# Kernel tuning notes

Measured on AMD Instinct MI355X. Metric: run time of the kernel, lower is better.

Reference implementation:

```python
import jax, jax.numpy as jnp
import numpy as np

NUM_USER = 50000
NUM_ITEM = 50000
NUM_NODES = NUM_USER + NUM_ITEM
DIM_LATENT = 256
DIM_ID = 64
NUM_EDGES = 2_000_000


def setup_inputs() -> dict:
    key = jax.random.key(0)
    ks = jax.random.split(key, 16)
    xn = lambda k, shape, s: (jax.random.normal(k, shape, dtype=jnp.float32) * s)
    # xavier-normal-ish std for [in,out] weights
    def xavier(k, fan_in, fan_out):
        std = float(np.sqrt(2.0 / (fan_in + fan_out)))
        return jax.random.normal(k, (fan_in, fan_out), dtype=jnp.float32) * std
    edge_index = jax.random.randint(ks[0], (2, NUM_EDGES), 0, NUM_NODES, dtype=jnp.int64)
    return {
        "features": xn(ks[1], (NUM_ITEM, DIM_LATENT), 1.0),
        "id_embedding": xn(ks[2], (NUM_NODES, DIM_ID), 1.0),
        "preference": xn(ks[3], (NUM_USER, DIM_LATENT), 0.1),
        "W_gcn0": xavier(ks[4], DIM_LATENT, DIM_ID),
        "W_gcn1": xavier(ks[5], DIM_ID, DIM_ID),
        "lin_w0": xavier(ks[6], DIM_LATENT, DIM_ID),
        "lin_b0": jnp.zeros((DIM_ID,), jnp.float32),
        "lin_w1": xavier(ks[7], DIM_ID, DIM_ID),
        "lin_b1": jnp.zeros((DIM_ID,), jnp.float32),
        "g_w0": xavier(ks[8], DIM_ID, DIM_ID),
        "g_b0": jnp.zeros((DIM_ID,), jnp.float32),
        "g_w1": xavier(ks[9], DIM_ID, DIM_ID),
        "g_b1": jnp.zeros((DIM_ID,), jnp.float32),
        "edge_index": edge_index,
    }


def _gcn(x, W, row, col, norm):
    # H = scatter_add(row, (x W)[col] * norm)
    h = x @ W                                  # [N, out]
    msg = h[col] * norm[:, None]               # [E, out] gather + scale
    return jax.ops.segment_sum(msg, row, num_segments=NUM_NODES)


def reference(features, id_embedding, preference, W_gcn0, W_gcn1,
              lin_w0, lin_b0, lin_w1, lin_b1, g_w0, g_b0, g_w1, g_b1,
              edge_index):
    row, col = edge_index[0], edge_index[1]
    # degree normalization: deg from scatter_add of ones over row
    deg = jax.ops.segment_sum(jnp.ones((row.shape[0],), jnp.float32), row,
                              num_segments=NUM_NODES)
    deg = jnp.maximum(deg, 1.0)
    dis = deg ** -0.5
    norm = dis[row] * dis[col]                 # [E]

    x = jnp.concatenate([preference, features], axis=0)   # [N, dim_latent]
    x = x / jnp.maximum(jnp.linalg.norm(x, axis=1, keepdims=True), 1e-12)

    lrelu = jax.nn.leaky_relu  # slope 0.01, matches torch default
    for W_gcn, lin_w, lin_b, g_w, g_b in (
        (W_gcn0, lin_w0, lin_b0, g_w0, g_b0),
        (W_gcn1, lin_w1, lin_b1, g_w1, g_b1),
    ):
        h = lrelu(_gcn(x, W_gcn, row, col, norm))          # [N, dim_id]
        x_hat = lrelu(x @ lin_w + lin_b) + id_embedding    # has_id=True
        x = lrelu(h @ g_w + g_b + x_hat)                   # concate=False
    return x
```

## Files before the change

kernel.cpp:

```cpp
#include <hip/hip_runtime.h>

#define NUM_USER   50000
#define NUM_ITEM   50000
#define NUM_NODES  100000
#define DIM_LATENT 256
#define DIM_ID     64
#define NUM_EDGES  2000000
#define NBUCKET    391
#define BPB        8192
#define NCHUNK     245
#define HSTRIDE    392

typedef __attribute__((ext_vector_type(8))) short bf8_t;
typedef __attribute__((ext_vector_type(4))) float f4_t;
typedef __attribute__((ext_vector_type(2))) float f2_t;

static __device__ __forceinline__ float lrelu(float x) {
    return x > 0.0f ? x : 0.01f * x;
}
static __device__ __forceinline__ unsigned short f2bf(float f) {
    unsigned u = __float_as_uint(f);
    u += 0x7fff + ((u >> 16) & 1);
    return (unsigned short)(u >> 16);
}
static __device__ __forceinline__ float bf2f(unsigned short u) {
    return __uint_as_float(((unsigned)u) << 16);
}
static __device__ __forceinline__ float bflo(unsigned u) {
    return __uint_as_float(u << 16);
}
static __device__ __forceinline__ float bfhi(unsigned u) {
    return __uint_as_float(u & 0xffff0000u);
}

__global__ void __launch_bounds__(256, 8) k_xnorm(const float* __restrict__ pref,
                                                  const float* __restrict__ feat,
                                                  unsigned short* __restrict__ xn) {
    const int w = threadIdx.x >> 6;
    const int lane = threadIdx.x & 63;
    const int n = blockIdx.x * 4 + w;
    const float* src = (n < NUM_USER) ? (pref + (size_t)n * DIM_LATENT)
                                      : (feat + (size_t)(n - NUM_USER) * DIM_LATENT);
    float4 v = reinterpret_cast<const float4*>(src)[lane];
    float ss = v.x*v.x + v.y*v.y + v.z*v.z + v.w*v.w;
    #pragma unroll
    for (int off = 32; off >= 1; off >>= 1) ss += __shfl_xor(ss, off);
    float sc = 1.0f / fmaxf(sqrtf(ss), 1e-12f);
    ushort4 p;
    p.x = f2bf(v.x * sc); p.y = f2bf(v.y * sc);
    p.z = f2bf(v.z * sc); p.w = f2bf(v.w * sc);
    *reinterpret_cast<ushort4*>(&xn[(size_t)n * DIM_LATENT + lane * 4]) = p;
}

__global__ void __launch_bounds__(256) k_hist(const int* __restrict__ row,
                                              int* __restrict__ hist) {
    __shared__ int lh[NBUCKET];
    const int g = blockIdx.x, t = threadIdx.x;
    for (int i = t; i < NBUCKET; i += 256) lh[i] = 0;
    __syncthreads();
    const int base = g * BPB;
    for (int i = 0; i < BPB; i += 256) {
        int e = base + i + t;
        if (e < NUM_EDGES) atomicAdd(&lh[row[e] >> 8], 1);
    }
    __syncthreads();
    for (int i = t; i < NBUCKET; i += 256) hist[g * HSTRIDE + i] = lh[i];
}

__global__ void __launch_bounds__(256) k_off1(int* __restrict__ hist,
                                              int* __restrict__ bcnt) {
    __shared__ int wsum[4];
    const int b = blockIdx.x, t = threadIdx.x;
    const int lane = t & 63, w = t >> 6;
    int c = (t < NCHUNK) ? hist[t * HSTRIDE + b] : 0;
    int v = c;
    #pragma unroll
    for (int off = 1; off < 64; off <<= 1) {
        int u = __shfl_up(v, off);
        if (lane >= off) v += u;
    }
    if (lane == 63) wsum[w] = v;
    __syncthreads();
    int add = 0;
    #pragma unroll
    for (int i = 0; i < 4; ++i) if (i < w) add += wsum[i];
    int incl = v + add;
    if (t < NCHUNK) hist[t * HSTRIDE + b] = incl - c;
    if (t == 255) bcnt[b] = incl;
}

__global__ void __launch_bounds__(512) k_bscan(const int* __restrict__ bcnt,
                                               int* __restrict__ boff) {
    __shared__ int wsum[8];
    const int t = threadIdx.x;
    const int lane = t & 63, w = t >> 6;
    int c = (t < NBUCKET) ? bcnt[t] : 0;
    int v = c;
    #pragma unroll
    for (int off = 1; off < 64; off <<= 1) {
        int u = __shfl_up(v, off);
        if (lane >= off) v += u;
    }
    if (lane == 63) wsum[w] = v;
    __syncthreads();
    int add = 0;
    #pragma unroll
    for (int i = 0; i < 8; ++i) if (i < w) add += wsum[i];
    int ex = v + add - c;
    if (t < NBUCKET) boff[t] = ex;
    if (t == NBUCKET - 1) boff[NBUCKET] = ex + c;
}

__global__ void __launch_bounds__(256) k_bin2(const int* __restrict__ row,
                                              const int* __restrict__ col,
                                              const int* __restrict__ hist,
                                              const int* __restrict__ boff,
                                              unsigned* __restrict__ epack) {
    __shared__ int curs[NBUCKET];
    const int g = blockIdx.x, t = threadIdx.x;
    for (int i = t; i < NBUCKET; i += 256) curs[i] = boff[i] + hist[g * HSTRIDE + i];
    __syncthreads();
    const int base = g * BPB;
    for (int i = 0; i < BPB; i += 256) {
        int e = base + i + t;
        if (e < NUM_EDGES) {
            int r = row[e];
            int pos = atomicAdd(&curs[r >> 8], 1);
            epack[pos] = ((unsigned)(r & 255) << 24) | (unsigned)col[e];
        }
    }
}

__global__ void __launch_bounds__(512) k_csr(const unsigned* __restrict__ epack,
                                             const int* __restrict__ boff,
                                             int* __restrict__ offs,
                                             int* __restrict__ cnt,
                                             float* __restrict__ dis,
                                             int* __restrict__ ecol) {
    __shared__ int lcnt[256];
    __shared__ int lofs[256];
    __shared__ int wsum[4];
    const int b = blockIdx.x, t = threadIdx.x;
    const int start = boff[b], end = boff[b + 1];
    if (t < 256) lcnt[t] = 0;
    __syncthreads();
    for (int e = start + t; e < end; e += 512)
        atomicAdd(&lcnt[epack[e] >> 24], 1);
    __syncthreads();

    const int lane = t & 63, w = t >> 6;
    int c = (t < 256) ? lcnt[t] : 0;
    int v = c;
    #pragma unroll
    for (int off = 1; off < 64; off <<= 1) {
        int u = __shfl_up(v, off);
        if (lane >= off) v += u;
    }
    if (t < 256 && lane == 63) wsum[w] = v;
    __syncthreads();
    if (t < 256) {
        int add = 0;
        #pragma unroll
        for (int i = 0; i < 4; ++i) if (i < w) add += wsum[i];
        int ex = v + add - c;
        lofs[t] = start + ex;
        int n = (b << 8) + t;
        if (n < NUM_NODES) {
            offs[n] = start + ex;
            cnt[n]  = c;
            dis[n]  = rsqrtf((float)max(c, 1));
        }
    }
    __syncthreads();
    for (int e = start + t; e < end; e += 512) {
        unsigned p = epack[e];
        int pos = atomicAdd(&lofs[p >> 24], 1);
        ecol[pos] = (int)(p & 0x00ffffffu);
    }
}

__global__ void __launch_bounds__(256) k_wprep(const float* __restrict__ Wg,
                                               const float* __restrict__ Wl,
                                               unsigned short* __restrict__ wfrag) {
    int g = blockIdx.x * 256 + threadIdx.x;
    if (g >= 4096) return;
    int ks = g >> 9;
    int t  = (g >> 6) & 7;
    int l  = g & 63;
    const float* W = (t < 4) ? Wg : Wl;
    int colg = (t & 3) * 16 + (l & 15);
    int kb = ks * 32 + (l >> 4) * 8;
    unsigned short o[8];
    #pragma unroll
    for (int e = 0; e < 8; ++e) o[e] = f2bf(W[(size_t)(kb + e) * DIM_ID + colg]);
    unsigned short* dst = wfrag + (size_t)g * 8;
    #pragma unroll
    for (int e = 0; e < 8; ++e) dst[e] = o[e];
}

__global__ void __launch_bounds__(256) k_wprep64(const float* __restrict__ W0,
                                                 const float* __restrict__ W1,
                                                 const float* __restrict__ W2,
                                                 const float* __restrict__ W3,
                                                 unsigned short* __restrict__ frag) {
    int g = blockIdx.x * 256 + threadIdx.x;
    if (g >= 2048) return;
    int m = g >> 9;
    int r = g & 511;
    int ks = r >> 8;
    int t  = (r >> 6) & 3;
    int l  = r & 63;
    const float* W = (m == 0) ? W0 : (m == 1) ? W1 : (m == 2) ? W2 : W3;
    int colg = t * 16 + (l & 15);
    int kb = ks * 32 + (l >> 4) * 8;
    unsigned short o[8];
    #pragma unroll
    for (int e = 0; e < 8; ++e) o[e] = f2bf(W[(size_t)(kb + e) * DIM_ID + colg]);
    unsigned short* dst = frag + (size_t)g * 8;
    #pragma unroll
    for (int e = 0; e < 8; ++e) dst[e] = o[e];
}

__global__ void __launch_bounds__(256, 3) k_l1(
    const unsigned short* __restrict__ xn,
    const unsigned short* __restrict__ wfrag,
    const float* __restrict__ lb,   const float* __restrict__ idemb,
    unsigned short* __restrict__ hbf, unsigned short* __restrict__ xhat)
{
    __shared__ unsigned short st[4][16][68];
    const int lane = threadIdx.x & 63;
    const int w = threadIdx.x >> 6;
    const int ql = lane & 15, q = lane >> 4;
    const int rowBase = (blockIdx.x * 4 + w) * 16;
    const int row = rowBase + ql;
    const unsigned short* src = xn + (size_t)((row < NUM_NODES) ? row : 0) * DIM_LATENT;

    bf8_t af[8];
    #pragma unroll
    for (int ks = 0; ks < 8; ++ks)
        af[ks] = *reinterpret_cast<const bf8_t*>(src + ks * 32 + q * 8);

    f4_t acc[8];
    #pragma unroll
    for (int t = 0; t < 8; ++t) acc[t] = (f4_t){0.f, 0.f, 0.f, 0.f};

    const bf8_t* wf = reinterpret_cast<const bf8_t*>(wfrag);
    #pragma unroll
    for (int ks = 0; ks < 8; ++ks) {
        #pragma unroll
        for (int t = 0; t < 8; ++t) {
            bf8_t b = wf[(ks * 8 + t) * 64 + lane];
            acc[t] = __builtin_amdgcn_mfma_f32_16x16x32_bf16(af[ks], b, acc[t], 0, 0, 0);
        }
    }

    #pragma unroll
    for (int t = 0; t < 4; ++t)
        #pragma unroll
        for (int reg = 0; reg < 4; ++reg)
            st[w][q * 4 + reg][t * 16 + ql] = f2bf(acc[t][reg]);
    #pragma unroll
    for (int it = 0; it < 4; ++it) {
        int i = it * 64 + lane;
        int r = i >> 4, c8 = i & 15;
        int n = rowBase + r;
        uint2 v = *reinterpret_cast<const uint2*>(&st[w][r][c8 * 4]);
        if (n < NUM_NODES)
            *reinterpret_cast<uint2*>(&hbf[(size_t)n * DIM_ID + c8 * 4]) = v;
    }

    #pragma unroll
    for (int t = 4; t < 8; ++t) {
        int colg = (t - 4) * 16 + ql;
        float lbl = lb[colg];
        #pragma unroll
        for (int reg = 0; reg < 4; ++reg)
            st[w][q * 4 + reg][colg] = f2bf(lrelu(acc[t][reg] + lbl));
    }
    #pragma unroll
    for (int it = 0; it < 4; ++it) {
        int i = it * 64 + lane;
        int r = i >> 4, c8 = i & 15;
        int n = rowBase + r;
        if (n < NUM_NODES) {
            uint2 s = *reinterpret_cast<const uint2*>(&st[w][r][c8 * 4]);
            float4 idv = *reinterpret_cast<const float4*>(&idemb[(size_t)n * DIM_ID + c8 * 4]);
            uint2 o;
            o.x = (unsigned)f2bf(bflo(s.x) + idv.x) | ((unsigned)f2bf(bfhi(s.x) + idv.y) << 16);
            o.y = (unsigned)f2bf(bflo(s.y) + idv.z) | ((unsigned)f2bf(bfhi(s.y) + idv.w) << 16);
            *reinterpret_cast<uint2*>(&xhat[(size_t)n * DIM_ID + c8 * 4]) = o;
        }
    }
}

__global__ void __launch_bounds__(256, 8) k_hcvt(const uint2* __restrict__ hp,
                                                 const float* __restrict__ dis,
                                                 unsigned* __restrict__ out) {
    int t = blockIdx.x * 256 + threadIdx.x;
    float dn = dis[t >> 4];
    uint2 u = hp[t];
    float v0 = bflo(u.x) * dn, v1 = bfhi(u.x) * dn;
    float v2 = bflo(u.y) * dn, v3 = bfhi(u.y) * dn;
    int p = __builtin_amdgcn_cvt_pk_fp8_f32(v0, v1, 0, false);
    p = __builtin_amdgcn_cvt_pk_fp8_f32(v2, v3, p, true);
    out[t] = (unsigned)p;
}

__global__ void __launch_bounds__(256, 8) k_hcvt1(const uint2* __restrict__ hp,
                                                  unsigned* __restrict__ out) {
    int t = blockIdx.x * 256 + threadIdx.x;
    uint2 u = hp[t];
    int p = __builtin_amdgcn_cvt_pk_fp8_f32(bflo(u.x), bfhi(u.x), 0, false);
    p = __builtin_amdgcn_cvt_pk_fp8_f32(bflo(u.y), bfhi(u.y), p, true);
    out[t] = (unsigned)p;
}

__global__ void __launch_bounds__(256, 8) k_gather(
    const unsigned char* __restrict__ hbf8, const float* __restrict__ dis,
    const int* __restrict__ offs, const int* __restrict__ cnt,
    const int* __restrict__ ecol, unsigned short* __restrict__ Hb)
{
    const int w = threadIdx.x >> 6;
    const int lane = threadIdx.x & 63;
    const int g = lane >> 3;
    const int k = lane & 7;
    const int n = blockIdx.x * 4 + w;

    const float dn = dis[n];
    const int start = offs[n];
    const int m = cnt[n];

    f2_t s01 = {0.f, 0.f}, s23 = {0.f, 0.f}, s45 = {0.f, 0.f}, s67 = {0.f, 0.f};

    for (int base = 0; base < m; base += 64) {
        int e = base + lane;
        int ec = (e < m) ? ecol[start + e] : 0;
        int lim = m - base; if (lim > 64) lim = 64;
        int nj = (lim + 7) >> 3;
        for (int jj = 0; jj < nj; jj += 4) {
            int i0 = jj * 8 + g, i1 = i0 + 8, i2 = i0 + 16, i3 = i0 + 24;
            int c0 = __shfl(ec, i0), c1 = __shfl(ec, i1);
            int c2 = __shfl(ec, i2), c3 = __shfl(ec, i3);
            uint2 u0 = make_uint2(0u,0u), u1 = make_uint2(0u,0u);
            uint2 u2 = make_uint2(0u,0u), u3 = make_uint2(0u,0u);
            if (i0 < lim) u0 = *reinterpret_cast<const uint2*>(hbf8 + (size_t)(c0 << 6) + (k << 3));
            if (i1 < lim) u1 = *reinterpret_cast<const uint2*>(hbf8 + (size_t)(c1 << 6) + (k << 3));
            if (i2 < lim) u2 = *reinterpret_cast<const uint2*>(hbf8 + (size_t)(c2 << 6) + (k << 3));
            if (i3 < lim) u3 = *reinterpret_cast<const uint2*>(hbf8 + (size_t)(c3 << 6) + (k << 3));
            s01 += __builtin_amdgcn_cvt_pk_f32_fp8(u0.x, false);
            s23 += __builtin_amdgcn_cvt_pk_f32_fp8(u0.x, true);
            s45 += __builtin_amdgcn_cvt_pk_f32_fp8(u0.y, false);
            s67 += __builtin_amdgcn_cvt_pk_f32_fp8(u0.y, true);
            s01 += __builtin_amdgcn_cvt_pk_f32_fp8(u1.x, false);
            s23 += __builtin_amdgcn_cvt_pk_f32_fp8(u1.x, true);
            s45 += __builtin_amdgcn_cvt_pk_f32_fp8(u1.y, false);
            s67 += __builtin_amdgcn_cvt_pk_f32_fp8(u1.y, true);
            s01 += __builtin_amdgcn_cvt_pk_f32_fp8(u2.x, false);
            s23 += __builtin_amdgcn_cvt_pk_f32_fp8(u2.x, true);
            s45 += __builtin_amdgcn_cvt_pk_f32_fp8(u2.y, false);
            s67 += __builtin_amdgcn_cvt_pk_f32_fp8(u2.y, true);
            s01 += __builtin_amdgcn_cvt_pk_f32_fp8(u3.x, false);
            s23 += __builtin_amdgcn_cvt_pk_f32_fp8(u3.x, true);
            s45 += __builtin_amdgcn_cvt_pk_f32_fp8(u3.y, false);
            s67 += __builtin_amdgcn_cvt_pk_f32_fp8(u3.y, true);
        }
    }
    float a0 = s01.x, a1 = s01.y, a2 = s23.x, a3 = s23.y;
    float a4 = s45.x, a5 = s45.y, a6 = s67.x, a7 = s67.y;
    #pragma unroll
    for (int off = 8; off <= 32; off <<= 1) {
        a0 += __shfl_xor(a0, off); a1 += __shfl_xor(a1, off);
        a2 += __shfl_xor(a2, off); a3 += __shfl_xor(a3, off);
        a4 += __shfl_xor(a4, off); a5 += __shfl_xor(a5, off);
        a6 += __shfl_xor(a6, off); a7 += __shfl_xor(a7, off);
    }
    if (lane < 8) {
        uint4 o;
        o.x = (unsigned)f2bf(a0 * dn) | ((unsigned)f2bf(a1 * dn) << 16);
        o.y = (unsigned)f2bf(a2 * dn) | ((unsigned)f2bf(a3 * dn) << 16);
        o.z = (unsigned)f2bf(a4 * dn) | ((unsigned)f2bf(a5 * dn) << 16);
        o.w = (unsigned)f2bf(a6 * dn) | ((unsigned)f2bf(a7 * dn) << 16);
        *reinterpret_cast<uint4*>(&Hb[(size_t)n * DIM_ID + lane * 8]) = o;
    }
}

__global__ void __launch_bounds__(256, 3) k_mid(
    const unsigned short* __restrict__ Hb, const unsigned short* __restrict__ xhat1,
    const unsigned short* __restrict__ wf64,
    const float* __restrict__ gb,  const float* __restrict__ lb1,
    const float* __restrict__ idemb, const float* __restrict__ dis,
    unsigned short* __restrict__ hbf, unsigned short* __restrict__ xhat2)
{
    __shared__ unsigned short x1s[4][16][DIM_ID];
    __shared__ unsigned short st[4][16][68];
    const int lane = threadIdx.x & 63;
    const int w = threadIdx.x >> 6;
    const int ql = lane & 15, q = lane >> 4;
    const int rowBase = (blockIdx.x * 4 + w) * 16;
    const int rowc = min(rowBase + ql, NUM_NODES - 1);

    bf8_t ha[2];
    #pragma unroll
    for (int ks = 0; ks < 2; ++ks) {
        uint4 u = *reinterpret_cast<const uint4*>(&Hb[(size_t)rowc * DIM_ID + ks * 32 + q * 8]);
        bf8_t a;
        a[0] = (short)f2bf(lrelu(bflo(u.x))); a[1] = (short)f2bf(lrelu(bfhi(u.x)));
        a[2] = (short)f2bf(lrelu(bflo(u.y))); a[3] = (short)f2bf(lrelu(bfhi(u.y)));
        a[4] = (short)f2bf(lrelu(bflo(u.z))); a[5] = (short)f2bf(lrelu(bfhi(u.z)));
        a[6] = (short)f2bf(lrelu(bflo(u.w))); a[7] = (short)f2bf(lrelu(bfhi(u.w)));
        ha[ks] = a;
    }

    const bf8_t* gw0f = reinterpret_cast<const bf8_t*>(wf64);
    f4_t acc1[4];
    #pragma unroll
    for (int t = 0; t < 4; ++t) acc1[t] = (f4_t){0.f, 0.f, 0.f, 0.f};
    #pragma unroll
    for (int ks = 0; ks < 2; ++ks)
        #pragma unroll
        for (int t = 0; t < 4; ++t)
            acc1[t] = __builtin_amdgcn_mfma_f32_16x16x32_bf16(ha[ks], gw0f[(ks * 4 + t) * 64 + lane], acc1[t], 0, 0, 0);

    int nn[4];
    #pragma unroll
    for (int reg = 0; reg < 4; ++reg) nn[reg] = rowBase + q * 4 + reg;

    #pragma unroll
    for (int t = 0; t < 4; ++t) {
        int colg = t * 16 + ql;
        float gbl = gb[colg];
        #pragma unroll
        for (int reg = 0; reg < 4; ++reg) {
            float xh = bf2f(xhat1[(size_t)min(nn[reg], NUM_NODES - 1) * DIM_ID + colg]);
            x1s[w][q * 4 + reg][colg] = f2bf(lrelu(acc1[t][reg] + gbl + xh));
        }
    }
    __syncthreads();

    bf8_t xa[2];
    #pragma unroll
    for (int ks = 0; ks < 2; ++ks)
        xa[ks] = *reinterpret_cast<const bf8_t*>(&x1s[w][ql][ks * 32 + q * 8]);

    const bf8_t* wg1f = reinterpret_cast<const bf8_t*>(wf64 + 512 * 8);
    const bf8_t* lw1f = reinterpret_cast<const bf8_t*>(wf64 + 1024 * 8);
    f4_t acc2[8];
    #pragma unroll
    for (int t = 0; t < 8; ++t) acc2[t] = (f4_t){0.f, 0.f, 0.f, 0.f};
    #pragma unroll
    for (int ks = 0; ks < 2; ++ks) {
        #pragma unroll
        for (int t = 0; t < 4; ++t)
            acc2[t] = __builtin_amdgcn_mfma_f32_16x16x32_bf16(xa[ks], wg1f[(ks * 4 + t) * 64 + lane], acc2[t], 0, 0, 0);
        #pragma unroll
        for (int t = 0; t < 4; ++t)
            acc2[4 + t] = __builtin_amdgcn_mfma_f32_16x16x32_bf16(xa[ks], lw1f[(ks * 4 + t) * 64 + lane], acc2[4 + t], 0, 0, 0);
    }

    float dn[4];
    #pragma unroll
    for (int reg = 0; reg < 4; ++reg)
        dn[reg] = (nn[reg] < NUM_NODES) ? dis[nn[reg]] : 0.0f;

    #pragma unroll
    for (int t = 0; t < 4; ++t)
        #pragma unroll
        for (int reg = 0; reg < 4; ++reg)
            st[w][q * 4 + reg][t * 16 + ql] = f2bf(acc2[t][reg] * dn[reg]);
    #pragma unroll
    for (int it = 0; it < 4; ++it) {
        int i = it * 64 + lane;
        int r = i >> 4, c8 = i & 15;
        int n = rowBase + r;
        uint2 v = *reinterpret_cast<const uint2*>(&st[w][r][c8 * 4]);
        if (n < NUM_NODES)
            *reinterpret_cast<uint2*>(&hbf[(size_t)n * DIM_ID + c8 * 4]) = v;
    }

    #pragma unroll
    for (int t = 0; t < 4; ++t) {
        int colg = t * 16 + ql;
        float lbl = lb1[colg];
        #pragma unroll
        for (int reg = 0; reg < 4; ++reg)
            st[w][q * 4 + reg][colg] = f2bf(lrelu(acc2[4 + t][reg] + lbl));
    }
    #pragma unroll
    for (int it = 0; it < 4; ++it) {
        int i = it * 64 + lane;
        int r = i >> 4, c8 = i & 15;
        int n = rowBase + r;
        if (n < NUM_NODES) {
            uint2 s = *reinterpret_cast<const uint2*>(&st[w][r][c8 * 4]);
            float4 idv = *reinterpret_cast<const float4*>(&idemb[(size_t)n * DIM_ID + c8 * 4]);
            uint2 o;
            o.x = (unsigned)f2bf(bflo(s.x) + idv.x) | ((unsigned)f2bf(bfhi(s.x) + idv.y) << 16);
            o.y = (unsigned)f2bf(bflo(s.y) + idv.z) | ((unsigned)f2bf(bfhi(s.y) + idv.w) << 16);
            *reinterpret_cast<uint2*>(&xhat2[(size_t)n * DIM_ID + c8 * 4]) = o;
        }
    }
}

__global__ void __launch_bounds__(256, 3) k_final(
    const unsigned short* __restrict__ Hb, const unsigned short* __restrict__ xhat,
    const unsigned short* __restrict__ wf64,
    const float* __restrict__ gb, float* __restrict__ out)
{
    const int lane = threadIdx.x & 63;
    const int w = threadIdx.x >> 6;
    const int ql = lane & 15, q = lane >> 4;
    const int rowBase = (blockIdx.x * 4 + w) * 16;
    const int rowc = min(rowBase + ql, NUM_NODES - 1);

    bf8_t ha[2];
    #pragma unroll
    for (int ks = 0; ks < 2; ++ks) {
        uint4 u = *reinterpret_cast<const uint4*>(&Hb[(size_t)rowc * DIM_ID + ks * 32 + q * 8]);
        bf8_t a;
        a[0] = (short)f2bf(lrelu(bflo(u.x))); a[1] = (short)f2bf(lrelu(bfhi(u.x)));
        a[2] = (short)f2bf(lrelu(bflo(u.y))); a[3] = (short)f2bf(lrelu(bfhi(u.y)));
        a[4] = (short)f2bf(lrelu(bflo(u.z))); a[5] = (short)f2bf(lrelu(bfhi(u.z)));
        a[6] = (short)f2bf(lrelu(bflo(u.w))); a[7] = (short)f2bf(lrelu(bfhi(u.w)));
        ha[ks] = a;
    }

    const bf8_t* gw1f = reinterpret_cast<const bf8_t*>(wf64 + 1536 * 8);
    f4_t acc[4];
    #pragma unroll
    for (int t = 0; t < 4; ++t) acc[t] = (f4_t){0.f, 0.f, 0.f, 0.f};
    #pragma unroll
    for (int ks = 0; ks < 2; ++ks)
        #pragma unroll
        for (int t = 0; t < 4; ++t)
            acc[t] = __builtin_amdgcn_mfma_f32_16x16x32_bf16(ha[ks], gw1f[(ks * 4 + t) * 64 + lane], acc[t], 0, 0, 0);

    int nn[4];
    #pragma unroll
    for (int reg = 0; reg < 4; ++reg) nn[reg] = rowBase + q * 4 + reg;

    #pragma unroll
    for (int t = 0; t < 4; ++t) {
        int colg = t * 16 + ql;
        float gbl = gb[colg];
        #pragma unroll
        for (int reg = 0; reg < 4; ++reg)
            if (nn[reg] < NUM_NODES) {
                size_t o = (size_t)nn[reg] * DIM_ID + colg;
                out[o] = lrelu(acc[t][reg] + gbl + bf2f(xhat[o]));
            }
    }
}

extern "C" void kernel_launch(void* const* d_in, const int* in_sizes, int n_in,
                              void* d_out, int out_size, void* d_ws, size_t ws_size,
                              hipStream_t stream)
{
    const float* features = (const float*)d_in[0];
    const float* idemb    = (const float*)d_in[1];
    const float* pref     = (const float*)d_in[2];
    const float* Wg0      = (const float*)d_in[3];
    const float* Wg1      = (const float*)d_in[4];
    const float* lw0      = (const float*)d_in[5];
    const float* lb0      = (const float*)d_in[6];
    const float* lw1      = (const float*)d_in[7];
    const float* lb1      = (const float*)d_in[8];
    const float* gw0      = (const float*)d_in[9];
    const float* gb0      = (const float*)d_in[10];
    const float* gw1      = (const float*)d_in[11];
    const float* gb1      = (const float*)d_in[12];
    const int*   edges    = (const int*)d_in[13];
    const int*   row      = edges;
    const int*   col      = edges + NUM_EDGES;

    char* ws = (char*)d_ws;
    int*      hist  = (int*)(ws + 0);
    int*      bcnt  = (int*)(ws + 524288);
    int*      boff  = (int*)(ws + 528384);
    int*      offs  = (int*)(ws + 532480);
    int*      cnt   = (int*)(ws + 1056768);
    float*    dis   = (float*)(ws + 1581056);
    unsigned short* wfrag = (unsigned short*)(ws + 2105344);
    unsigned short* wf64  = (unsigned short*)(ws + 2170880);
    unsigned short* xn    = (unsigned short*)(ws + 2236416);
    int*      ecol  = (int*)(ws + 2236416);
    unsigned* epack = (unsigned*)(ws + 10625024);
    unsigned short* Hbf   = (unsigned short*)(ws + 19013632);
    unsigned char*  hbf8  = (unsigned char*)(ws + 32000000);
    unsigned short* hbf   = (unsigned short*)(ws + 53436416);
    unsigned short* xhatb = (unsigned short*)(ws + 66236416);
    float* out   = (float*)d_out;

    const int l1Blocks = (NUM_NODES + 63) / 64;
    const int gatherBlocks = NUM_NODES / 4;
    const int cvtBlocks = NUM_NODES * 16 / 256;

    k_wprep<<<16, 256, 0, stream>>>(Wg0, lw0, wfrag);
    k_wprep64<<<8, 256, 0, stream>>>(gw0, Wg1, lw1, gw1, wf64);
    k_xnorm<<<NUM_NODES / 4, 256, 0, stream>>>(pref, features, xn);
    k_hist<<<NCHUNK, 256, 0, stream>>>(row, hist);
    k_off1<<<NBUCKET, 256, 0, stream>>>(hist, bcnt);
    k_bscan<<<1, 512, 0, stream>>>(bcnt, boff);

    k_l1<<<l1Blocks, 256, 0, stream>>>(xn, wfrag, lb0, idemb, hbf, xhatb);

    k_bin2<<<NCHUNK, 256, 0, stream>>>(row, col, hist, boff, epack);
    k_csr<<<NBUCKET, 512, 0, stream>>>(epack, boff, offs, cnt, dis, ecol);
    k_hcvt<<<cvtBlocks, 256, 0, stream>>>((const uint2*)hbf, dis, (unsigned*)hbf8);

    k_gather<<<gatherBlocks, 256, 0, stream>>>(hbf8, dis, offs, cnt, ecol, Hbf);

    k_mid<<<l1Blocks, 256, 0, stream>>>(Hbf, xhatb, wf64, gb0, lb1, idemb, dis,
                                        hbf, xhatb);
    k_hcvt1<<<cvtBlocks, 256, 0, stream>>>((const uint2*)hbf, (unsigned*)hbf8);

    k_gather<<<gatherBlocks, 256, 0, stream>>>(hbf8, dis, offs, cnt, ecol, Hbf);
    k_final<<<l1Blocks, 256, 0, stream>>>(Hbf, xhatb, wf64, gb1, out);
}
```

Measured before the change: 235.0 us.

## Fuse front-end kernels, compute degrees early, write fp8 directly from GEMM kernels

Merges the normalization, histogram and a new global-atomic degree count into one heterogeneous launch. The bucket-binning pass now runs as extra blocks inside the layer-1 GEMM launch, and degree scaling moves into that GEMM epilogue. The GEMM and mid kernels write fp8 directly, which removes the two standalone conversion kernels. This cuts launch count, intermediate bf16 round-trips and serialization, at the cost of 2M global atomics for the degree count and an extra memset.

Result: slower. 286.6 us (+21.9%).

```diff
diff --git a/kernel.cpp b/kernel.cpp
--- a/kernel.cpp
+++ b/kernel.cpp
@@ -10,6 +10,9 @@
 #define BPB        8192
 #define NCHUNK     245
 #define HSTRIDE    392
+#define XN_BLOCKS  25000
+#define DEG_BLOCKS 7813
+#define L1_BLOCKS  1563
 
 typedef __attribute__((ext_vector_type(8))) short bf8_t;
 typedef __attribute__((ext_vector_type(4))) float f4_t;
@@ -32,46 +35,63 @@
 static __device__ __forceinline__ float bfhi(unsigned u) {
     return __uint_as_float(u & 0xffff0000u);
 }
-
-__global__ void __launch_bounds__(256, 8) k_xnorm(const float* __restrict__ pref,
-                                                  const float* __restrict__ feat,
-                                                  unsigned short* __restrict__ xn) {
-    const int w = threadIdx.x >> 6;
-    const int lane = threadIdx.x & 63;
-    const int n = blockIdx.x * 4 + w;
-    const float* src = (n < NUM_USER) ? (pref + (size_t)n * DIM_LATENT)
-                                      : (feat + (size_t)(n - NUM_USER) * DIM_LATENT);
-    float4 v = reinterpret_cast<const float4*>(src)[lane];
-    float ss = v.x*v.x + v.y*v.y + v.z*v.z + v.w*v.w;
-    #pragma unroll
-    for (int off = 32; off >= 1; off >>= 1) ss += __shfl_xor(ss, off);
-    float sc = 1.0f / fmaxf(sqrtf(ss), 1e-12f);
-    ushort4 p;
-    p.x = f2bf(v.x * sc); p.y = f2bf(v.y * sc);
-    p.z = f2bf(v.z * sc); p.w = f2bf(v.w * sc);
-    *reinterpret_cast<ushort4*>(&xn[(size_t)n * DIM_LATENT + lane * 4]) = p;
-}
-
-__global__ void __launch_bounds__(256) k_hist(const int* __restrict__ row,
-                                              int* __restrict__ hist) {
+static __device__ __forceinline__ f2_t shfl2(f2_t v, int off) {
+    long long l = __shfl_xor(__builtin_bit_cast(long long, v), off);
+    return __builtin_bit_cast(f2_t, l);
+}
+
+__global__ void __launch_bounds__(256, 8) k_front(
+    const float* __restrict__ pref, const float* __restrict__ feat,
+    const int* __restrict__ row,
+    unsigned short* __restrict__ xn, int* __restrict__ hist,
+    int* __restrict__ cnt2)
+{
     __shared__ int lh[NBUCKET];
-    const int g = blockIdx.x, t = threadIdx.x;
-    for (int i = t; i < NBUCKET; i += 256) lh[i] = 0;
-    __syncthreads();
-    const int base = g * BPB;
-    for (int i = 0; i < BPB; i += 256) {
-        int e = base + i + t;
-        if (e < NUM_EDGES) atomicAdd(&lh[row[e] >> 8], 1);
-    }
-    __syncthreads();
-    for (int i = t; i < NBUCKET; i += 256) hist[g * HSTRIDE + i] = lh[i];
+    const int b = blockIdx.x, t = threadIdx.x;
+
+    if (b < XN_BLOCKS) {
+        const int w = t >> 6;
+        const int lane = t & 63;
+        const int n = b * 4 + w;
+        const float* src = (n < NUM_USER) ? (pref + (size_t)n * DIM_LATENT)
+                                          : (feat + (size_t)(n - NUM_USER) * DIM_LATENT);
+        float4 v = reinterpret_cast<const float4*>(src)[lane];
+        float ss = v.x*v.x + v.y*v.y + v.z*v.z + v.w*v.w;
+        #pragma unroll
+        for (int off = 32; off >= 1; off >>= 1) ss += __shfl_xor(ss, off);
+        float sc = 1.0f / fmaxf(sqrtf(ss), 1e-12f);
+        ushort4 p;
+        p.x = f2bf(v.x * sc); p.y = f2bf(v.y * sc);
+        p.z = f2bf(v.z * sc); p.w = f2bf(v.w * sc);
+        *reinterpret_cast<ushort4*>(&xn[(size_t)n * DIM_LATENT + lane * 4]) = p;
+    } else if (b < XN_BLOCKS + NCHUNK) {
+        const int g = b - XN_BLOCKS;
+        for (int i = t; i < NBUCKET; i += 256) lh[i] = 0;
+        __syncthreads();
+        const int base = g * BPB;
+        for (int i = 0; i < BPB; i += 256) {
+            int e = base + i + t;
+            if (e < NUM_EDGES) atomicAdd(&lh[row[e] >> 8], 1);
+        }
+        __syncthreads();
+        for (int i = t; i < NBUCKET; i += 256) hist[g * HSTRIDE + i] = lh[i];
+    } else {
+        int e = (b - XN_BLOCKS - NCHUNK) * 256 + t;
+        if (e < NUM_EDGES) atomicAdd(&cnt2[row[e]], 1);
+    }
 }
 
 __global__ void __launch_bounds__(256) k_off1(int* __restrict__ hist,
-                                              int* __restrict__ bcnt) {
+                                              int* __restrict__ bcnt,
+                                              const int* __restrict__ cnt2,
+                                              float* __restrict__ dis) {
     __shared__ int wsum[4];
     const int b = blockIdx.x, t = threadIdx.x;
     const int lane = t & 63, w = t >> 6;
+
+    int n = (b << 8) + t;
+    if (n < NUM_NODES) dis[n] = rsqrtf((float)max(cnt2[n], 1));
+
     int c = (t < NCHUNK) ? hist[t * HSTRIDE + b] : 0;
     int v = c;
     #pragma unroll
@@ -109,74 +129,6 @@
     int ex = v + add - c;
     if (t < NBUCKET) boff[t] = ex;
     if (t == NBUCKET - 1) boff[NBUCKET] = ex + c;
-}
-
-__global__ void __launch_bounds__(256) k_bin2(const int* __restrict__ row,
-                                              const int* __restrict__ col,
-                                              const int* __restrict__ hist,
-                                              const int* __restrict__ boff,
-                                              unsigned* __restrict__ epack) {
-    __shared__ int curs[NBUCKET];
-    const int g = blockIdx.x, t = threadIdx.x;
-    for (int i = t; i < NBUCKET; i += 256) curs[i] = boff[i] + hist[g * HSTRIDE + i];
-    __syncthreads();
-    const int base = g * BPB;
-    for (int i = 0; i < BPB; i += 256) {
-        int e = base + i + t;
-        if (e < NUM_EDGES) {
-            int r = row[e];
-            int pos = atomicAdd(&curs[r >> 8], 1);
-            epack[pos] = ((unsigned)(r & 255) << 24) | (unsigned)col[e];
-        }
-    }
-}
-
-__global__ void __launch_bounds__(512) k_csr(const unsigned* __restrict__ epack,
-                                             const int* __restrict__ boff,
-                                             int* __restrict__ offs,
-                                             int* __restrict__ cnt,
-                                             float* __restrict__ dis,
-                                             int* __restrict__ ecol) {
-    __shared__ int lcnt[256];
-    __shared__ int lofs[256];
-    __shared__ int wsum[4];
-    const int b = blockIdx.x, t = threadIdx.x;
-    const int start = boff[b], end = boff[b + 1];
-    if (t < 256) lcnt[t] = 0;
-    __syncthreads();
-    for (int e = start + t; e < end; e += 512)
-        atomicAdd(&lcnt[epack[e] >> 24], 1);
-    __syncthreads();
-
-    const int lane = t & 63, w = t >> 6;
-    int c = (t < 256) ? lcnt[t] : 0;
-    int v = c;
-    #pragma unroll
-    for (int off = 1; off < 64; off <<= 1) {
-        int u = __shfl_up(v, off);
-        if (lane >= off) v += u;
-    }
-    if (t < 256 && lane == 63) wsum[w] = v;
-    __syncthreads();
-    if (t < 256) {
-        int add = 0;
-        #pragma unroll
-        for (int i = 0; i < 4; ++i) if (i < w) add += wsum[i];
-        int ex = v + add - c;
-        lofs[t] = start + ex;
-        int n = (b << 8) + t;
-        if (n < NUM_NODES) {
-            offs[n] = start + ex;
-            cnt[n]  = c;
-            dis[n]  = rsqrtf((float)max(c, 1));
-        }
-    }
-    __syncthreads();
-    for (int e = start + t; e < end; e += 512) {
-        unsigned p = epack[e];
-        int pos = atomicAdd(&lofs[p >> 24], 1);
-        ecol[pos] = (int)(p & 0x00ffffffu);
-    }
 }
 
 __global__ void __launch_bounds__(256) k_wprep(const float* __restrict__ Wg,
@@ -221,19 +173,42 @@
     for (int e = 0; e < 8; ++e) dst[e] = o[e];
 }
 
-__global__ void __launch_bounds__(256, 3) k_l1(
+__global__ void __launch_bounds__(256, 3) k_l1bin(
     const unsigned short* __restrict__ xn,
     const unsigned short* __restrict__ wfrag,
     const float* __restrict__ lb,   const float* __restrict__ idemb,
-    unsigned short* __restrict__ hbf, unsigned short* __restrict__ xhat)
+    const float* __restrict__ dis,
+    unsigned char* __restrict__ hbf8, unsigned short* __restrict__ xhat,
+    const int* __restrict__ row, const int* __restrict__ col,
+    const int* __restrict__ hist, const int* __restrict__ boff,
+    unsigned* __restrict__ epack)
 {
     __shared__ unsigned short st[4][16][68];
+    __shared__ int curs[NBUCKET];
+    const int blk = blockIdx.x;
+
+    if (blk >= L1_BLOCKS) {
+        const int g = blk - L1_BLOCKS, t = threadIdx.x;
+        for (int i = t; i < NBUCKET; i += 256) curs[i] = boff[i] + hist[g * HSTRIDE + i];
+        __syncthreads();
+        const int base = g * BPB;
+        for (int i = 0; i < BPB; i += 256) {
+            int e = base + i + t;
+            if (e < NUM_EDGES) {
+                int r = row[e];
+                int pos = atomicAdd(&curs[r >> 8], 1);
+                epack[pos] = ((unsigned)(r & 255) << 24) | (unsigned)col[e];
+            }
+        }
+        return;
+    }
+
     const int lane = threadIdx.x & 63;
     const int w = threadIdx.x >> 6;
     const int ql = lane & 15, q = lane >> 4;
-    const int rowBase = (blockIdx.x * 4 + w) * 16;
-    const int row = rowBase + ql;
-    const unsigned short* src = xn + (size_t)((row < NUM_NODES) ? row : 0) * DIM_LATENT;
+    const int rowBase = (blk * 4 + w) * 16;
+    const int rown = rowBase + ql;
+    const unsigned short* src = xn + (size_t)((rown < NUM_NODES) ? rown : 0) * DIM_LATENT;
 
     bf8_t af[8];
     #pragma unroll
@@ -254,19 +229,30 @@
         }
     }
 
+    int nn[4];
+    float dn[4];
+    #pragma unroll
+    for (int reg = 0; reg < 4; ++reg) {
+        nn[reg] = rowBase + q * 4 + reg;
+        dn[reg] = (nn[reg] < NUM_NODES) ? dis[nn[reg]] : 0.0f;
+    }
+
     #pragma unroll
     for (int t = 0; t < 4; ++t)
         #pragma unroll
         for (int reg = 0; reg < 4; ++reg)
-            st[w][q * 4 + reg][t * 16 + ql] = f2bf(acc[t][reg]);
+            st[w][q * 4 + reg][t * 16 + ql] = f2bf(acc[t][reg] * dn[reg]);
     #pragma unroll
     for (int it = 0; it < 4; ++it) {
         int i = it * 64 + lane;
         int r = i >> 4, c8 = i & 15;
         int n = rowBase + r;
-        uint2 v = *reinterpret_cast<const uint2*>(&st[w][r][c8 * 4]);
-        if (n < NUM_NODES)
-            *reinterpret_cast<uint2*>(&hbf[(size_t)n * DIM_ID + c8 * 4]) = v;
+        uint2 s = *reinterpret_cast<const uint2*>(&st[w][r][c8 * 4]);
+        if (n < NUM_NODES) {
+            int p = __builtin_amdgcn_cvt_pk_fp8_f32(bflo(s.x), bfhi(s.x), 0, false);
+            p = __builtin_amdgcn_cvt_pk_fp8_f32(bflo(s.y), bfhi(s.y), p, true);
+            *reinterpret_cast<unsigned*>(hbf8 + (size_t)n * DIM_ID + c8 * 4) = (unsigned)p;
+        }
     }
 
     #pragma unroll
@@ -293,26 +279,46 @@
     }
 }
 
-__global__ void __launch_bounds__(256, 8) k_hcvt(const uint2* __restrict__ hp,
-                                                 const float* __restrict__ dis,
-                                                 unsigned* __restrict__ out) {
-    int t = blockIdx.x * 256 + threadIdx.x;
-    float dn = dis[t >> 4];
-    uint2 u = hp[t];
-    float v0 = bflo(u.x) * dn, v1 = bfhi(u.x) * dn;
-    float v2 = bflo(u.y) * dn, v3 = bfhi(u.y) * dn;
-    int p = __builtin_amdgcn_cvt_pk_fp8_f32(v0, v1, 0, false);
-    p = __builtin_amdgcn_cvt_pk_fp8_f32(v2, v3, p, true);
-    out[t] = (unsigned)p;
-}
-
-__global__ void __launch_bounds__(256, 8) k_hcvt1(const uint2* __restrict__ hp,
-                                                  unsigned* __restrict__ out) {
-    int t = blockIdx.x * 256 + threadIdx.x;
-    uint2 u = hp[t];
-    int p = __builtin_amdgcn_cvt_pk_fp8_f32(bflo(u.x), bfhi(u.x), 0, false);
-    p = __builtin_amdgcn_cvt_pk_fp8_f32(bflo(u.y), bfhi(u.y), p, true);
-    out[t] = (unsigned)p;
+__global__ void __launch_bounds__(512) k_csr(const unsigned* __restrict__ epack,
+                                             const int* __restrict__ boff,
+                                             int* __restrict__ offs,
+                                             int* __restrict__ ecol) {
+    __shared__ int lcnt[256];
+    __shared__ int lofs[256];
+    __shared__ int wsum[4];
+    const int b = blockIdx.x, t = threadIdx.x;
+    const int start = boff[b], end = boff[b + 1];
+    if (t < 256) lcnt[t] = 0;
+    __syncthreads();
+    for (int e = start + t; e < end; e += 512)
+        atomicAdd(&lcnt[epack[e] >> 24], 1);
+    __syncthreads();
+
+    const int lane = t & 63, w = t >> 6;
+    int c = (t < 256) ? lcnt[t] : 0;
+    int v = c;
+    #pragma unroll
+    for (int off = 1; off < 64; off <<= 1) {
+        int u = __shfl_up(v, off);
+        if (lane >= off) v += u;
+    }
+    if (t < 256 && lane == 63) wsum[w] = v;
+    __syncthreads();
+    if (t < 256) {
+        int add = 0;
+        #pragma unroll
+        for (int i = 0; i < 4; ++i) if (i < w) add += wsum[i];
+        int ex = v + add - c;
+        lofs[t] = start + ex;
+        int n = (b << 8) + t;
+        if (n < NUM_NODES) offs[n] = start + ex;
+    }
+    __syncthreads();
+    for (int e = start + t; e < end; e += 512) {
+        unsigned p = epack[e];
+        int pos = atomicAdd(&lofs[p >> 24], 1);
+        ecol[pos] = (int)(p & 0x00ffffffu);
+    }
 }
 
 __global__ void __launch_bounds__(256, 8) k_gather(
@@ -365,21 +371,19 @@
             s67 += __builtin_amdgcn_cvt_pk_f32_fp8(u3.y, true);
         }
     }
-    float a0 = s01.x, a1 = s01.y, a2 = s23.x, a3 = s23.y;
-    float a4 = s45.x, a5 = s45.y, a6 = s67.x, a7 = s67.y;
     #pragma unroll
     for (int off = 8; off <= 32; off <<= 1) {
-        a0 += __shfl_xor(a0, off); a1 += __shfl_xor(a1, off);
-        a2 += __shfl_xor(a2, off); a3 += __shfl_xor(a3, off);
-        a4 += __shfl_xor(a4, off); a5 += __shfl_xor(a5, off);
-        a6 += __shfl_xor(a6, off); a7 += __shfl_xor(a7, off);
+        s01 += shfl2(s01, off);
+        s23 += shfl2(s23, off);
+        s45 += shfl2(s45, off);
+        s67 += shfl2(s67, off);
     }
     if (lane < 8) {
         uint4 o;
-        o.x = (unsigned)f2bf(a0 * dn) | ((unsigned)f2bf(a1 * dn) << 16);
-        o.y = (unsigned)f2bf(a2 * dn) | ((unsigned)f2bf(a3 * dn) << 16);
-        o.z = (unsigned)f2bf(a4 * dn) | ((unsigned)f2bf(a5 * dn) << 16);
-        o.w = (unsigned)f2bf(a6 * dn) | ((unsigned)f2bf(a7 * dn) << 16);
+        o.x = (unsigned)f2bf(s01.x * dn) | ((unsigned)f2bf(s01.y * dn) << 16);
+        o.y = (unsigned)f2bf(s23.x * dn) | ((unsigned)f2bf(s23.y * dn) << 16);
+        o.z = (unsigned)f2bf(s45.x * dn) | ((unsigned)f2bf(s45.y * dn) << 16);
+        o.w = (unsigned)f2bf(s67.x * dn) | ((unsigned)f2bf(s67.y * dn) << 16);
         *reinterpret_cast<uint4*>(&Hb[(size_t)n * DIM_ID + lane * 8]) = o;
     }
 }
@@ -389,7 +393,7 @@
     const unsigned short* __restrict__ wf64,
     const float* __restrict__ gb,  const float* __restrict__ lb1,
     const float* __restrict__ idemb, const float* __restrict__ dis,
-    unsigned short* __restrict__ hbf, unsigned short* __restrict__ xhat2)
+    unsigned char* __restrict__ hbf8, unsigned short* __restrict__ xhat2)
 {
     __shared__ unsigned short x1s[4][16][DIM_ID];
     __shared__ unsigned short st[4][16][68];
@@ -472,9 +476,12 @@
         int i = it * 64 + lane;
         int r = i >> 4, c8 = i & 15;
         int n = rowBase + r;
-        uint2 v = *reinterpret_cast<const uint2*>(&st[w][r][c8 * 4]);
-        if (n < NUM_NODES)
-            *reinterpret_cast<uint2*>(&hbf[(size_t)n * DIM_ID + c8 * 4]) = v;
+        uint2 s = *reinterpret_cast<const uint2*>(&st[w][r][c8 * 4]);
+        if (n < NUM_NODES) {
+            int p = __builtin_amdgcn_cvt_pk_fp8_f32(bflo(s.x), bfhi(s.x), 0, false);
+            p = __builtin_amdgcn_cvt_pk_fp8_f32(bflo(s.y), bfhi(s.y), p, true);
+            *reinterpret_cast<unsigned*>(hbf8 + (size_t)n * DIM_ID + c8 * 4) = (unsigned)p;
+        }
     }
 
     #pragma unroll
@@ -577,42 +584,39 @@
     int*      bcnt  = (int*)(ws + 524288);
     int*      boff  = (int*)(ws + 528384);
     int*      offs  = (int*)(ws + 532480);
-    int*      cnt   = (int*)(ws + 1056768);
+    int*      cnt2  = (int*)(ws + 1056768);
     float*    dis   = (float*)(ws + 1581056);
     unsigned short* wfrag = (unsigned short*)(ws + 2105344);
     unsigned short* wf64  = (unsigned short*)(ws + 2170880);
     unsigned short* xn    = (unsigned short*)(ws + 2236416);
     int*      ecol  = (int*)(ws + 2236416);
-    unsigned* epack = (unsigned*)(ws + 10625024);
-    unsigned short* Hbf   = (unsigned short*)(ws + 19013632);
-    unsigned char*  hbf8  = (unsigned char*)(ws + 32000000);
-    unsigned short* hbf   = (unsigned short*)(ws + 53436416);
-    unsigned short* xhatb = (unsigned short*)(ws + 66236416);
+    unsigned short* Hbf = (unsigned short*)(ws + 19013632);
+    unsigned* epack = (unsigned*)(ws + 53436416);
+    unsigned char*  hbf8  = (unsigned char*)(ws + 61436416);
+    unsigned short* xhatb = (unsigned short*)(ws + 67836416);
     float* out   = (float*)d_out;
 
-    const int l1Blocks = (NUM_NODES + 63) / 64;
     const int gatherBlocks = NUM_NODES / 4;
-    const int cvtBlocks = NUM_NODES * 16 / 256;
-
+    const int frontBlocks = XN_BLOCKS + NCHUNK + DEG_BLOCKS;
+    const int k2Blocks = L1_BLOCKS + NCHUNK;
+
+    hipMemsetAsync(cnt2, 0, NUM_NODES * sizeof(int), stream);
     k_wprep<<<16, 256, 0, stream>>>(Wg0, lw0, wfrag);
     k_wprep64<<<8, 256, 0, stream>>>(gw0, Wg1, lw1, gw1, wf64);
-    k_xnorm<<<NUM_NODES / 4, 256, 0, stream>>>(pref, features, xn);
-    k_hist<<<NCHUNK, 256, 0, stream>>>(row, hist);
-    k_off1<<<NBUCKET, 256, 0, stream>>>(hist, bcnt);
+
+    k_front<<<frontBlocks, 256, 0, stream>>>(pref, features, row, xn, hist, cnt2);
+    k_off1<<<NBUCKET, 256, 0, stream>>>(hist, bcnt, cnt2, dis);
     k_bscan<<<1, 512, 0, stream>>>(bcnt, boff);
 
-    k_l1<<<l1Blocks, 256, 0, stream>>>(xn, wfrag, lb0, idemb, hbf, xhatb);
-
-    k_bin2<<<NCHUNK, 256, 0, stream>>>(row, col, hist, boff, epack);
-    k_csr<<<NBUCKET, 512, 0, stream>>>(epack, boff, offs, cnt, dis, ecol);
-    k_hcvt<<<cvtBlocks, 256, 0, stream>>>((const uint2*)hbf, dis, (unsigned*)hbf8);
-
-    k_gather<<<gatherBlocks, 256, 0, stream>>>(hbf8, dis, offs, cnt, ecol, Hbf);
-
-    k_mid<<<l1Blocks, 256, 0, stream>>>(Hbf, xhatb, wf64, gb0, lb1, idemb, dis,
-                                        hbf, xhatb);
-    k_hcvt1<<<cvtBlocks, 256, 0, stream>>>((const uint2*)hbf, (unsigned*)hbf8);
-
-    k_gather<<<gatherBlocks, 256, 0, stream>>>(hbf8, dis, offs, cnt, ecol, Hbf);
-    k_final<<<l1Blocks, 256, 0, stream>>>(Hbf, xhatb, wf64, gb1, out);
-}
+    k_l1bin<<<k2Blocks, 256, 0, stream>>>(xn, wfrag, lb0, idemb, dis, hbf8, xhatb,
+                                          row, col, hist, boff, epack);
+    k_csr<<<NBUCKET, 512, 0, stream>>>(epack, boff, offs, ecol);
+
+    k_gather<<<gatherBlocks, 256, 0, stream>>>(hbf8, dis, offs, cnt2, ecol, Hbf);
+
+    k_mid<<<L1_BLOCKS, 256, 0, stream>>>(Hbf, xhatb, wf64, gb0, lb1, idemb, dis,
+                                         hbf8, xhatb);
+
+    k_gather<<<gatherBlocks, 256, 0, stream>>>(hbf8, dis, offs, cnt2, ecol, Hbf);
+    k_final<<<L1_BLOCKS, 256, 0, stream>>>(Hbf, xhatb, wf64, gb1, out);
+}
```
